# Kernel optimization log

Measured on AMD Instinct MI355X. Metric: run time of the kernel, lower is better.

## Reference

```python
import jax, jax.numpy as jnp
import numpy as np

K = 9  # kernel_size ** 2
G = 4  # groups
POINTS = np.array([[-1, -1], [-1, 0], [-1, 1], [0, -1], [0, 0], [0, 1], [1, -1], [1, 0], [1, 1]], dtype=np.float32)


def conv2d(x, w, b=None, pad=0):
    out = jax.lax.conv_general_dilated(x, w, (1, 1), [(pad, pad), (pad, pad)],
                                       dimension_numbers=('NCHW', 'OIHW', 'NCHW'))
    if b is not None:
        out = out + b[None, :, None, None]
    return out


def pconv(z, w):
    # partial conv: 3x3 conv on first dim//4 channels, rest untouched
    dc = w.shape[0]
    z1 = conv2d(z[:, :dc], w, pad=1)
    return jnp.concatenate([z1, z[:, dc:]], axis=1)


def warp(img, flow):
    # img: (b, Cg, H, W); flow: (b, 2K, H, W) -> (b, Cg, K, H, W)
    # bilinear grid_sample, padding_mode='border', align_corners=True
    b, Cg, H, W = img.shape
    fl = flow.reshape(b, K, 2, H, W)
    gy, gx = jnp.meshgrid(jnp.arange(H, dtype=img.dtype), jnp.arange(W, dtype=img.dtype), indexing='ij')
    px = jnp.clip(gx[None, None] + fl[:, :, 0], 0.0, W - 1)  # (b, K, H, W)
    py = jnp.clip(gy[None, None] + fl[:, :, 1], 0.0, H - 1)
    x0 = jnp.floor(px)
    y0 = jnp.floor(py)
    wx = (px - x0)[:, None]  # (b, 1, K, H, W)
    wy = (py - y0)[:, None]
    x0i = x0.astype(jnp.int32)
    y0i = y0.astype(jnp.int32)
    x1i = jnp.minimum(x0i + 1, W - 1)
    y1i = jnp.minimum(y0i + 1, H - 1)
    gather = jax.vmap(lambda im, iy, ix: im[:, iy, ix])  # per-batch: (Cg,H,W),(K,H,W)->(Cg,K,H,W)
    v00 = gather(img, y0i, x0i)
    v01 = gather(img, y0i, x1i)
    v10 = gather(img, y1i, x0i)
    v11 = gather(img, y1i, x1i)
    return v00 * (1 - wx) * (1 - wy) + v01 * wx * (1 - wy) + v10 * (1 - wx) * wy + v11 * wx * wy


def forward(x, y, off_pconv_w, off_w, off_b, mask_pconv_w, mask_w, mask_b):
    mask = conv2d(pconv(x, mask_pconv_w), mask_w, mask_b)[:, None]  # (b, 1, K, h, w)
    y1, y2 = jnp.split(y, 2, axis=0)
    Cg = y1.shape[1] // G
    pts = jnp.asarray(POINTS).astype(x.dtype)
    outs1, outs2 = [], []
    for i in range(G):
        base = (pts * (2 * i + 1)).reshape(-1)  # (2K,) base offsets at scale 2i+1
        off = conv2d(pconv(x, off_pconv_w[i]), off_w[i], off_b[i]) + base[None, :, None, None]
        outs1.append(warp(y1[:, i * Cg:(i + 1) * Cg], off) * mask)
        outs2.append(warp(y2[:, i * Cg:(i + 1) * Cg], off) * mask)
    return jnp.concatenate([jnp.concatenate(outs1, 1), jnp.concatenate(outs2, 1)], axis=0)


def setup_inputs() -> dict:
    key = jax.random.key(0)
    ks = jax.random.split(key, 8)
    b, inc, H, W = 2, 64, 256, 256
    dc = inc // 4
    return {
        'x': jax.random.normal(ks[0], (b, inc, H, W), jnp.float32),
        'y': jax.random.normal(ks[1], (2 * b, inc, H, W), jnp.float32),
        'off_pconv_w': jax.random.normal(ks[2], (G, dc, dc, 3, 3), jnp.float32) * 0.05,
        'off_w': jax.random.normal(ks[3], (G, 2 * K, inc, 1, 1), jnp.float32) * 0.05,
        'off_b': jax.random.normal(ks[4], (G, 2 * K), jnp.float32) * 0.05,
        'mask_pconv_w': jax.random.normal(ks[5], (dc, dc, 3, 3), jnp.float32) * 0.05,
        'mask_w': jax.random.normal(ks[6], (K, inc, 1, 1), jnp.float32) * 0.05,
        'mask_b': jax.random.normal(ks[7], (K,), jnp.float32) * 0.05,
    }


def reference(x, y, off_pconv_w, off_w, off_b, mask_pconv_w, mask_w, mask_b):
    return forward(x, y, off_pconv_w, off_w, off_b, mask_pconv_w, mask_w, mask_b)
```

## Files before the change

### kernel.cpp

```cpp
#include <hip/hip_runtime.h>

#define HW 65536
#define NOUT 81
#define NFEAT 192
#define WROW 84

typedef unsigned short ushort_t;
typedef unsigned int uint_t;

__device__ __forceinline__ float bf2f(ushort_t u) {
    union { unsigned int i; float f; } v; v.i = ((unsigned int)u) << 16; return v.f;
}
__device__ __forceinline__ float bfhi(uint_t u) {
    union { unsigned int i; float f; } v; v.i = u & 0xffff0000u; return v.f;
}
__device__ __forceinline__ float bflo(uint_t u) {
    union { unsigned int i; float f; } v; v.i = u << 16; return v.f;
}
__device__ __forceinline__ ushort_t f2bf(float f) {
    union { float f; unsigned int i; } v; v.f = f;
    unsigned int r = v.i + 0x7FFF + ((v.i >> 16) & 1);
    return (ushort_t)(r >> 16);
}

__global__ __launch_bounds__(256) void setup_weights(
    const float* __restrict__ off_pconv_w,
    const float* __restrict__ off_w,
    const float* __restrict__ off_b,
    const float* __restrict__ mask_pconv_w,
    const float* __restrict__ mask_w,
    const float* __restrict__ mask_b,
    float* __restrict__ WtP,
    float* __restrict__ biasP)
{
    int id = blockIdx.x * 256 + threadIdx.x;
    const float PTS[18] = {-1,-1, -1,0, -1,1, 0,-1, 0,0, 0,1, 1,-1, 1,0, 1,1};
    if (id < NFEAT * WROW) {
        int f = id / WROW;
        int o = id % WROW;
        float v = 0.f;
        if (o < NOUT) {
            if (f < 144) {
                int p = f >> 4, c = f & 15;
                float s = 0.f;
                if (o < 9) {
                    for (int cm = 0; cm < 16; ++cm)
                        s += mask_w[o * 64 + cm] * mask_pconv_w[(cm * 16 + c) * 9 + p];
                } else {
                    int oo = o - 9, i = oo / 18, j = oo % 18;
                    for (int cm = 0; cm < 16; ++cm)
                        s += off_w[(i * 18 + j) * 64 + cm] * off_pconv_w[((i * 16 + cm) * 16 + c) * 9 + p];
                }
                v = s;
            } else {
                int c = f - 144;
                if (o < 9) v = mask_w[o * 64 + 16 + c];
                else { int oo = o - 9, i = oo / 18, j = oo % 18; v = off_w[(i * 18 + j) * 64 + 16 + c]; }
            }
        }
        WtP[id] = v;
    } else if (id < NFEAT * WROW + NOUT) {
        int o = id - NFEAT * WROW;
        float v;
        if (o < 9) v = mask_b[o];
        else {
            int oo = o - 9, i = oo / 18, j = oo % 18;
            v = off_b[i * 18 + j] + PTS[j] * (float)(2 * i + 1);
        }
        biasP[o] = v;
    }
}

#define FMA21X4(X0, X1, X2, X3, WR) do {                                   \
    _Pragma("unroll")                                                      \
    for (int j5 = 0; j5 < 5; ++j5) {                                       \
        float4 w4 = *(const float4*)((WR) + 4 * j5);                       \
        acc0[4*j5+0] = fmaf(X0, w4.x, acc0[4*j5+0]);                       \
        acc0[4*j5+1] = fmaf(X0, w4.y, acc0[4*j5+1]);                       \
        acc0[4*j5+2] = fmaf(X0, w4.z, acc0[4*j5+2]);                       \
        acc0[4*j5+3] = fmaf(X0, w4.w, acc0[4*j5+3]);                       \
        acc1[4*j5+0] = fmaf(X1, w4.x, acc1[4*j5+0]);                       \
        acc1[4*j5+1] = fmaf(X1, w4.y, acc1[4*j5+1]);                       \
        acc1[4*j5+2] = fmaf(X1, w4.z, acc1[4*j5+2]);                       \
        acc1[4*j5+3] = fmaf(X1, w4.w, acc1[4*j5+3]);                       \
        acc2[4*j5+0] = fmaf(X2, w4.x, acc2[4*j5+0]);                       \
        acc2[4*j5+1] = fmaf(X2, w4.y, acc2[4*j5+1]);                       \
        acc2[4*j5+2] = fmaf(X2, w4.z, acc2[4*j5+2]);                       \
        acc2[4*j5+3] = fmaf(X2, w4.w, acc2[4*j5+3]);                       \
        acc3[4*j5+0] = fmaf(X3, w4.x, acc3[4*j5+0]);                       \
        acc3[4*j5+1] = fmaf(X3, w4.y, acc3[4*j5+1]);                       \
        acc3[4*j5+2] = fmaf(X3, w4.z, acc3[4*j5+2]);                       \
        acc3[4*j5+3] = fmaf(X3, w4.w, acc3[4*j5+3]);                       \
    }                                                                      \
    {                                                                      \
        float w20 = (WR)[20];                                              \
        acc0[20] = fmaf(X0, w20, acc0[20]);                                \
        acc1[20] = fmaf(X1, w20, acc1[20]);                                \
        acc2[20] = fmaf(X2, w20, acc2[20]);                                \
        acc3[20] = fmaf(X3, w20, acc3[20]);                                \
    }                                                                      \
} while (0)

__global__ __launch_bounds__(256, 2) void conv_px4(
    const float* __restrict__ x,
    const float* __restrict__ WtP,
    const float* __restrict__ biasP,
    float* __restrict__ mask_ws,
    float* __restrict__ off_ws)
{
    __shared__ float wl[NFEAT * WROW];
    int tid = threadIdx.x;
    {
        const float4* src = (const float4*)WtP;
        float4* dst = (float4*)wl;
        for (int idx = tid; idx < NFEAT * WROW / 4; idx += 256) dst[idx] = src[idx];
    }
    __syncthreads();

    int c4 = tid & 3, grp = tid >> 2;
    int bid = blockIdx.x;
    int b = bid >> 8, h = bid & 255;
    int wbase = grp * 4;
    int pix0 = h * 256 + wbase;
    int ob0 = c4 * 20;

    float acc0[21], acc1[21], acc2[21], acc3[21];
#pragma unroll
    for (int j = 0; j < 21; ++j) {
        float bj = biasP[ob0 + j];
        acc0[j] = bj; acc1[j] = bj; acc2[j] = bj; acc3[j] = bj;
    }

    const float* xb = x + (size_t)b * 64 * HW;

#pragma unroll 1
    for (int r = 0; r < 3; ++r) {
        int hh = h + r - 1;
        bool vrow = ((unsigned)hh < 256u);
        int rbase = hh * 256 + wbase;
#pragma unroll 1
        for (int c = 0; c < 16; ++c) {
            const float* xr = xb + c * HW + rbase;
            float4 x4 = vrow ? *(const float4*)xr : make_float4(0.f, 0.f, 0.f, 0.f);
            float xm1 = (vrow && wbase > 0)       ? xr[-1] : 0.f;
            float xp4 = (vrow && wbase + 4 < 256) ? xr[4]  : 0.f;
            const float* wr0 = wl + ((r * 3 + 0) * 16 + c) * WROW + ob0;
            const float* wr1 = wl + ((r * 3 + 1) * 16 + c) * WROW + ob0;
            const float* wr2 = wl + ((r * 3 + 2) * 16 + c) * WROW + ob0;
            FMA21X4(xm1, x4.x, x4.y, x4.z, wr0);
            FMA21X4(x4.x, x4.y, x4.z, x4.w, wr1);
            FMA21X4(x4.y, x4.z, x4.w, xp4, wr2);
        }
    }
#pragma unroll 1
    for (int c = 0; c < 48; ++c) {
        float4 x4 = *(const float4*)(xb + (16 + c) * HW + pix0);
        const float* wr = wl + (144 + c) * WROW + ob0;
        FMA21X4(x4.x, x4.y, x4.z, x4.w, wr);
    }

#pragma unroll
    for (int j = 0; j < 21; ++j) {
        int o = ob0 + j;
        float* pl;
        if (o < 9) pl = mask_ws + (size_t)(b * 9 + o) * HW + pix0;
        else       pl = off_ws  + (size_t)(b * 72 + (o - 9)) * HW + pix0;
        pl[0] = acc0[j];
        pl[1] = acc1[j];
        pl[2] = acc2[j];
        pl[3] = acc3[j];
    }
}

__global__ __launch_bounds__(256) void transpose_y_c(
    const float* __restrict__ y, ushort_t* __restrict__ Tc)
{
    int bid = blockIdx.x;
    int z = bid & 7, pr = bid >> 3;
    int pix = pr * 256 + threadIdx.x;
    int xb = z >> 2, i = z & 3;

    const float* p0 = y + (size_t)(xb * 64 + i * 16) * HW + pix;
    const float* p1 = y + (size_t)((xb + 2) * 64 + i * 16) * HW + pix;

    ushort_t v0[16], v1[16];
#pragma unroll
    for (int c = 0; c < 16; ++c) v0[c] = f2bf(p0[(size_t)c * HW]);
#pragma unroll
    for (int c = 0; c < 16; ++c) v1[c] = f2bf(p1[(size_t)c * HW]);

    uint4* dst = (uint4*)(Tc + ((size_t)z * HW + pix) * 32);
#pragma unroll
    for (int j = 0; j < 4; ++j) {
        ushort_t row[8] = {v0[4*j], v0[4*j+1], v0[4*j+2], v0[4*j+3],
                           v1[4*j], v1[4*j+1], v1[4*j+2], v1[4*j+3]};
        dst[j] = *(const uint4*)row;
    }
}

__global__ __launch_bounds__(256) void warp_apply_c(
    const ushort_t* __restrict__ Tc,
    const float* __restrict__ mask_ws,
    const float* __restrict__ off_ws,
    float* __restrict__ out)
{
    int bid = blockIdx.x;
    int z  = bid & 7;
    int wc = (bid >> 3) & 3;
    int h  = bid >> 5;
    int c4 = threadIdx.x & 3;
    int pl = threadIdx.x >> 2;
    int w  = wc * 64 + pl;
    int pix = h * 256 + w;
    int xb = z >> 2, i = z & 3;

    const ushort_t* Tt = Tc + (size_t)z * HW * 32;

    float oxv[9], oyv[9], mv[9];
#pragma unroll
    for (int k = 0; k < 9; ++k) {
        oxv[k] = off_ws[(size_t)(z * 18 + 2 * k) * HW + pix];
        oyv[k] = off_ws[(size_t)(z * 18 + 2 * k + 1) * HW + pix];
        mv[k]  = mask_ws[(size_t)(xb * 9 + k) * HW + pix];
    }

    float* ob0 = out + ((size_t)(xb * 64 + i * 16 + c4 * 4)) * 9 * HW + pix;
    float* ob1 = ob0 + (size_t)128 * 9 * HW;
    int sec = c4 * 8;

#pragma unroll 1
    for (int k = 0; k < 9; ++k) {
        float m = mv[k];
        float px = fminf(fmaxf((float)w + oxv[k], 0.f), 255.f);
        float py = fminf(fmaxf((float)h + oyv[k], 0.f), 255.f);
        float x0f = floorf(px), y0f = floorf(py);
        float wx = px - x0f, wy = py - y0f;
        int x0 = (int)x0f, y0 = (int)y0f;
        int x1 = min(x0 + 1, 255), y1 = min(y0 + 1, 255);

        float w00 = (1.f - wx) * (1.f - wy) * m;
        float w01 = wx * (1.f - wy) * m;
        float w10 = (1.f - wx) * wy * m;
        float w11 = wx * wy * m;

        uint4 A = *(const uint4*)(Tt + (size_t)(y0 * 256 + x0) * 32 + sec);
        uint4 B = *(const uint4*)(Tt + (size_t)(y0 * 256 + x1) * 32 + sec);
        uint4 C = *(const uint4*)(Tt + (size_t)(y1 * 256 + x0) * 32 + sec);
        uint4 D = *(const uint4*)(Tt + (size_t)(y1 * 256 + x1) * 32 + sec);

        float s0 = w00 * bflo(A.x), s1 = w00 * bfhi(A.x);
        float s2 = w00 * bflo(A.y), s3 = w00 * bfhi(A.y);
        float u0 = w00 * bflo(A.z), u1 = w00 * bfhi(A.z);
        float u2 = w00 * bflo(A.w), u3 = w00 * bfhi(A.w);

        s0 = fmaf(w01, bflo(B.x), s0); s1 = fmaf(w01, bfhi(B.x), s1);
        s2 = fmaf(w01, bflo(B.y), s2); s3 = fmaf(w01, bfhi(B.y), s3);
        u0 = fmaf(w01, bflo(B.z), u0); u1 = fmaf(w01, bfhi(B.z), u1);
        u2 = fmaf(w01, bflo(B.w), u2); u3 = fmaf(w01, bfhi(B.w), u3);

        s0 = fmaf(w10, bflo(C.x), s0); s1 = fmaf(w10, bfhi(C.x), s1);
        s2 = fmaf(w10, bflo(C.y), s2); s3 = fmaf(w10, bfhi(C.y), s3);
        u0 = fmaf(w10, bflo(C.z), u0); u1 = fmaf(w10, bfhi(C.z), u1);
        u2 = fmaf(w10, bflo(C.w), u2); u3 = fmaf(w10, bfhi(C.w), u3);

        s0 = fmaf(w11, bflo(D.x), s0); s1 = fmaf(w11, bfhi(D.x), s1);
        s2 = fmaf(w11, bflo(D.y), s2); s3 = fmaf(w11, bfhi(D.y), s3);
        u0 = fmaf(w11, bflo(D.z), u0); u1 = fmaf(w11, bfhi(D.z), u1);
        u2 = fmaf(w11, bflo(D.w), u2); u3 = fmaf(w11, bfhi(D.w), u3);

        float* p0 = ob0 + (size_t)k * HW;
        __builtin_nontemporal_store(s0, p0);
        __builtin_nontemporal_store(s1, p0 + (size_t)9 * HW);
        __builtin_nontemporal_store(s2, p0 + (size_t)18 * HW);
        __builtin_nontemporal_store(s3, p0 + (size_t)27 * HW);
        float* p1 = ob1 + (size_t)k * HW;
        __builtin_nontemporal_store(u0, p1);
        __builtin_nontemporal_store(u1, p1 + (size_t)9 * HW);
        __builtin_nontemporal_store(u2, p1 + (size_t)18 * HW);
        __builtin_nontemporal_store(u3, p1 + (size_t)27 * HW);
    }
}

__global__ __launch_bounds__(512) void conv_offsets_lds(
    const float* __restrict__ x, const float* __restrict__ WtP,
    const float* __restrict__ biasP,
    float* __restrict__ mask_ws, float* __restrict__ off_ws)
{
    __shared__ float wl[NFEAT * WROW + NOUT];
    int tid = threadIdx.x;
    for (int idx = tid; idx < NFEAT * WROW; idx += 512) wl[idx] = WtP[idx];
    if (tid < NOUT) wl[NFEAT * WROW + tid] = biasP[tid];
    __syncthreads();

    int gid = blockIdx.x * 512 + tid;
    int b = gid >> 16;
    int pix = gid & 65535;
    int h = pix >> 8, w = pix & 255;

    float acc[NOUT];
#pragma unroll
    for (int o = 0; o < NOUT; ++o) acc[o] = wl[NFEAT * WROW + o];

    const float* xb = x + (size_t)b * 64 * HW;
    for (int p = 0; p < 9; ++p) {
        int hh = h + p / 3 - 1;
        int ww = w + p % 3 - 1;
        bool valid = ((unsigned)hh < 256u) && ((unsigned)ww < 256u);
        int poff = hh * 256 + ww;
        for (int c = 0; c < 16; ++c) {
            float xv = valid ? xb[c * HW + poff] : 0.f;
            const float* wr = &wl[(p * 16 + c) * WROW];
#pragma unroll
            for (int o = 0; o < NOUT; ++o) acc[o] = fmaf(xv, wr[o], acc[o]);
        }
    }
    for (int c = 0; c < 48; ++c) {
        float xv = xb[(16 + c) * HW + pix];
        const float* wr = &wl[(144 + c) * WROW];
#pragma unroll
        for (int o = 0; o < NOUT; ++o) acc[o] = fmaf(xv, wr[o], acc[o]);
    }
#pragma unroll
    for (int k = 0; k < 9; ++k) mask_ws[(b * 9 + k) * HW + pix] = acc[k];
#pragma unroll
    for (int t = 0; t < 72; ++t) off_ws[(b * 72 + t) * HW + pix] = acc[9 + t];
}

__global__ __launch_bounds__(256) void warp_apply(
    const float* __restrict__ y,
    const float* __restrict__ mask_ws,
    const float* __restrict__ off_ws,
    float* __restrict__ out)
{
    int w = threadIdx.x;
    int h = blockIdx.x;
    int k = blockIdx.y;
    int z = blockIdx.z;
    int xb = z >> 2, i = z & 3;
    int pix = h * 256 + w;

    float ox = off_ws[(size_t)(z * 18 + 2 * k) * HW + pix];
    float oy = off_ws[(size_t)(z * 18 + 2 * k + 1) * HW + pix];
    float m  = mask_ws[(size_t)(xb * 9 + k) * HW + pix];

    float px = fminf(fmaxf((float)w + ox, 0.f), 255.f);
    float py = fminf(fmaxf((float)h + oy, 0.f), 255.f);
    float x0f = floorf(px), y0f = floorf(py);
    float wx = px - x0f, wy = py - y0f;
    int x0 = (int)x0f, y0 = (int)y0f;
    int x1 = min(x0 + 1, 255), y1 = min(y0 + 1, 255);

    float w00 = (1.f - wx) * (1.f - wy) * m;
    float w01 = wx * (1.f - wy) * m;
    float w10 = (1.f - wx) * wy * m;
    float w11 = wx * wy * m;

    int o00 = y0 * 256 + x0, o01 = y0 * 256 + x1;
    int o10 = y1 * 256 + x0, o11 = y1 * 256 + x1;

    const float* p1 = y + (size_t)(xb * 64 + i * 16) * HW;
    const float* p2 = y + (size_t)((xb + 2) * 64 + i * 16) * HW;
    float* out1 = out + ((size_t)(xb * 64 + i * 16) * 9 + k) * HW + pix;
    float* out2 = out + ((size_t)((xb + 2) * 64 + i * 16) * 9 + k) * HW + pix;

#pragma unroll
    for (int c = 0; c < 16; ++c) {
        const float* q = p1 + (size_t)c * HW;
        float v = w00 * q[o00] + w01 * q[o01] + w10 * q[o10] + w11 * q[o11];
        out1[(size_t)c * 9 * HW] = v;
        q = p2 + (size_t)c * HW;
        v = w00 * q[o00] + w01 * q[o01] + w10 * q[o10] + w11 * q[o11];
        out2[(size_t)c * 9 * HW] = v;
    }
}

extern "C" void kernel_launch(void* const* d_in, const int* in_sizes, int n_in,
                              void* d_out, int out_size, void* d_ws, size_t ws_size,
                              hipStream_t stream) {
    const float* x            = (const float*)d_in[0];
    const float* y            = (const float*)d_in[1];
    const float* off_pconv_w  = (const float*)d_in[2];
    const float* off_w        = (const float*)d_in[3];
    const float* off_b        = (const float*)d_in[4];
    const float* mask_pconv_w = (const float*)d_in[5];
    const float* mask_w       = (const float*)d_in[6];
    const float* mask_b       = (const float*)d_in[7];
    float* out = (float*)d_out;

    float* WtP     = (float*)d_ws;
    float* biasP   = WtP + NFEAT * WROW;
    float* mask_ws = (float*)((char*)d_ws + 65536);
    float* off_ws  = mask_ws + (size_t)2 * 9 * HW;
    ushort_t* Tc   = (ushort_t*)(off_ws + (size_t)2 * 72 * HW);
    size_t need = 65536 + (size_t)2 * 9 * HW * 4 + (size_t)2 * 72 * HW * 4
                + (size_t)8 * HW * 32 * 2;

    setup_weights<<<64, 256, 0, stream>>>(off_pconv_w, off_w, off_b,
                                          mask_pconv_w, mask_w, mask_b, WtP, biasP);

    if (ws_size >= need) {
        conv_px4<<<512, 256, 0, stream>>>(x, WtP, biasP, mask_ws, off_ws);
        transpose_y_c<<<2048, 256, 0, stream>>>(y, Tc);
        warp_apply_c<<<8192, 256, 0, stream>>>(Tc, mask_ws, off_ws, out);
    } else {
        conv_offsets_lds<<<256, 512, 0, stream>>>(x, WtP, biasP, mask_ws, off_ws);
        dim3 g2(256, 9, 8);
        warp_apply<<<g2, 256, 0, stream>>>(y, mask_ws, off_ws, out);
    }
}
```

Baseline: 299.6 us.

## Replace LDS-tiled offset conv with wave-uniform scalar-load weight conv

Replaces the conv kernel, which staged weights in LDS and gave each thread 4 pixels × 21 outputs, with one where each wavefront handles 64 pixels and a wave-uniform 21-output slice. The slice index goes through readfirstlane so the compiler can read weights from global memory with scalar loads. This drops the LDS staging, the barrier and LDS read traffic, and raises occupancy through smaller register use. In exchange each input pixel is loaded four times, once per output slice wave, with no float4 reuse across neighbouring pixels. The unused LDS fallback conv kernel is removed.

```diff
diff --git a/kernel.cpp b/kernel.cpp
--- a/kernel.cpp
+++ b/kernel.cpp
@@ -8,9 +8,6 @@
 typedef unsigned short ushort_t;
 typedef unsigned int uint_t;
 
-__device__ __forceinline__ float bf2f(ushort_t u) {
-    union { unsigned int i; float f; } v; v.i = ((unsigned int)u) << 16; return v.f;
-}
 __device__ __forceinline__ float bfhi(uint_t u) {
     union { unsigned int i; float f; } v; v.i = u & 0xffff0000u; return v.f;
 }
@@ -71,104 +68,59 @@
     }
 }
 
-#define FMA21X4(X0, X1, X2, X3, WR) do {                                   \
-    _Pragma("unroll")                                                      \
-    for (int j5 = 0; j5 < 5; ++j5) {                                       \
-        float4 w4 = *(const float4*)((WR) + 4 * j5);                       \
-        acc0[4*j5+0] = fmaf(X0, w4.x, acc0[4*j5+0]);                       \
-        acc0[4*j5+1] = fmaf(X0, w4.y, acc0[4*j5+1]);                       \
-        acc0[4*j5+2] = fmaf(X0, w4.z, acc0[4*j5+2]);                       \
-        acc0[4*j5+3] = fmaf(X0, w4.w, acc0[4*j5+3]);                       \
-        acc1[4*j5+0] = fmaf(X1, w4.x, acc1[4*j5+0]);                       \
-        acc1[4*j5+1] = fmaf(X1, w4.y, acc1[4*j5+1]);                       \
-        acc1[4*j5+2] = fmaf(X1, w4.z, acc1[4*j5+2]);                       \
-        acc1[4*j5+3] = fmaf(X1, w4.w, acc1[4*j5+3]);                       \
-        acc2[4*j5+0] = fmaf(X2, w4.x, acc2[4*j5+0]);                       \
-        acc2[4*j5+1] = fmaf(X2, w4.y, acc2[4*j5+1]);                       \
-        acc2[4*j5+2] = fmaf(X2, w4.z, acc2[4*j5+2]);                       \
-        acc2[4*j5+3] = fmaf(X2, w4.w, acc2[4*j5+3]);                       \
-        acc3[4*j5+0] = fmaf(X3, w4.x, acc3[4*j5+0]);                       \
-        acc3[4*j5+1] = fmaf(X3, w4.y, acc3[4*j5+1]);                       \
-        acc3[4*j5+2] = fmaf(X3, w4.z, acc3[4*j5+2]);                       \
-        acc3[4*j5+3] = fmaf(X3, w4.w, acc3[4*j5+3]);                       \
-    }                                                                      \
-    {                                                                      \
-        float w20 = (WR)[20];                                              \
-        acc0[20] = fmaf(X0, w20, acc0[20]);                                \
-        acc1[20] = fmaf(X1, w20, acc1[20]);                                \
-        acc2[20] = fmaf(X2, w20, acc2[20]);                                \
-        acc3[20] = fmaf(X3, w20, acc3[20]);                                \
-    }                                                                      \
-} while (0)
-
-__global__ __launch_bounds__(256, 2) void conv_px4(
+__global__ __launch_bounds__(256) void conv_sgpr(
     const float* __restrict__ x,
     const float* __restrict__ WtP,
     const float* __restrict__ biasP,
     float* __restrict__ mask_ws,
     float* __restrict__ off_ws)
 {
-    __shared__ float wl[NFEAT * WROW];
     int tid = threadIdx.x;
-    {
-        const float4* src = (const float4*)WtP;
-        float4* dst = (float4*)wl;
-        for (int idx = tid; idx < NFEAT * WROW / 4; idx += 256) dst[idx] = src[idx];
-    }
-    __syncthreads();
-
-    int c4 = tid & 3, grp = tid >> 2;
+    int lane = tid & 63;
     int bid = blockIdx.x;
-    int b = bid >> 8, h = bid & 255;
-    int wbase = grp * 4;
-    int pix0 = h * 256 + wbase;
-    int ob0 = c4 * 20;
-
-    float acc0[21], acc1[21], acc2[21], acc3[21];
-#pragma unroll
-    for (int j = 0; j < 21; ++j) {
-        float bj = biasP[ob0 + j];
-        acc0[j] = bj; acc1[j] = bj; acc2[j] = bj; acc3[j] = bj;
-    }
+    int b = bid >> 10;
+    int pixblk = (bid & 1023) * 64;
+    int pix = pixblk + lane;
+    int h = pix >> 8, w = pix & 255;
+
+    int ob0 = __builtin_amdgcn_readfirstlane((tid >> 6) * 20);
+
+    float acc[21];
+#pragma unroll
+    for (int j = 0; j < 21; ++j) acc[j] = biasP[ob0 + j];
 
     const float* xb = x + (size_t)b * 64 * HW;
 
 #pragma unroll 1
-    for (int r = 0; r < 3; ++r) {
-        int hh = h + r - 1;
-        bool vrow = ((unsigned)hh < 256u);
-        int rbase = hh * 256 + wbase;
+    for (int p = 0; p < 9; ++p) {
+        int hh = h + p / 3 - 1;
+        int dx = p % 3 - 1;
+        int ww = w + dx;
+        bool valid = ((unsigned)hh < 256u) && ((unsigned)ww < 256u);
+        int poff = hh * 256 + ww;
 #pragma unroll 1
         for (int c = 0; c < 16; ++c) {
-            const float* xr = xb + c * HW + rbase;
-            float4 x4 = vrow ? *(const float4*)xr : make_float4(0.f, 0.f, 0.f, 0.f);
-            float xm1 = (vrow && wbase > 0)       ? xr[-1] : 0.f;
-            float xp4 = (vrow && wbase + 4 < 256) ? xr[4]  : 0.f;
-            const float* wr0 = wl + ((r * 3 + 0) * 16 + c) * WROW + ob0;
-            const float* wr1 = wl + ((r * 3 + 1) * 16 + c) * WROW + ob0;
-            const float* wr2 = wl + ((r * 3 + 2) * 16 + c) * WROW + ob0;
-            FMA21X4(xm1, x4.x, x4.y, x4.z, wr0);
-            FMA21X4(x4.x, x4.y, x4.z, x4.w, wr1);
-            FMA21X4(x4.y, x4.z, x4.w, xp4, wr2);
+            float xv = valid ? xb[c * HW + poff] : 0.f;
+            const float* wr = WtP + (p * 16 + c) * WROW + ob0;
+#pragma unroll
+            for (int j = 0; j < 21; ++j) acc[j] = fmaf(xv, wr[j], acc[j]);
         }
     }
 #pragma unroll 1
     for (int c = 0; c < 48; ++c) {
-        float4 x4 = *(const float4*)(xb + (16 + c) * HW + pix0);
-        const float* wr = wl + (144 + c) * WROW + ob0;
-        FMA21X4(x4.x, x4.y, x4.z, x4.w, wr);
+        float xv = xb[(16 + c) * HW + pix];
+        const float* wr = WtP + (144 + c) * WROW + ob0;
+#pragma unroll
+        for (int j = 0; j < 21; ++j) acc[j] = fmaf(xv, wr[j], acc[j]);
     }
 
 #pragma unroll
     for (int j = 0; j < 21; ++j) {
         int o = ob0 + j;
         float* pl;
-        if (o < 9) pl = mask_ws + (size_t)(b * 9 + o) * HW + pix0;
-        else       pl = off_ws  + (size_t)(b * 72 + (o - 9)) * HW + pix0;
-        pl[0] = acc0[j];
-        pl[1] = acc1[j];
-        pl[2] = acc2[j];
-        pl[3] = acc3[j];
+        if (o < 9) pl = mask_ws + (size_t)(b * 9 + o) * HW + pix;
+        else       pl = off_ws  + (size_t)(b * 72 + (o - 9)) * HW + pix;
+        *pl = acc[j];
     }
 }
 
@@ -279,51 +231,6 @@
         __builtin_nontemporal_store(u2, p1 + (size_t)18 * HW);
         __builtin_nontemporal_store(u3, p1 + (size_t)27 * HW);
     }
-}
-
-__global__ __launch_bounds__(512) void conv_offsets_lds(
-    const float* __restrict__ x, const float* __restrict__ WtP,
-    const float* __restrict__ biasP,
-    float* __restrict__ mask_ws, float* __restrict__ off_ws)
-{
-    __shared__ float wl[NFEAT * WROW + NOUT];
-    int tid = threadIdx.x;
-    for (int idx = tid; idx < NFEAT * WROW; idx += 512) wl[idx] = WtP[idx];
-    if (tid < NOUT) wl[NFEAT * WROW + tid] = biasP[tid];
-    __syncthreads();
-
-    int gid = blockIdx.x * 512 + tid;
-    int b = gid >> 16;
-    int pix = gid & 65535;
-    int h = pix >> 8, w = pix & 255;
-
-    float acc[NOUT];
-#pragma unroll
-    for (int o = 0; o < NOUT; ++o) acc[o] = wl[NFEAT * WROW + o];
-
-    const float* xb = x + (size_t)b * 64 * HW;
-    for (int p = 0; p < 9; ++p) {
-        int hh = h + p / 3 - 1;
-        int ww = w + p % 3 - 1;
-        bool valid = ((unsigned)hh < 256u) && ((unsigned)ww < 256u);
-        int poff = hh * 256 + ww;
-        for (int c = 0; c < 16; ++c) {
-            float xv = valid ? xb[c * HW + poff] : 0.f;
-            const float* wr = &wl[(p * 16 + c) * WROW];
-#pragma unroll
-            for (int o = 0; o < NOUT; ++o) acc[o] = fmaf(xv, wr[o], acc[o]);
-        }
-    }
-    for (int c = 0; c < 48; ++c) {
-        float xv = xb[(16 + c) * HW + pix];
-        const float* wr = &wl[(144 + c) * WROW];
-#pragma unroll
-        for (int o = 0; o < NOUT; ++o) acc[o] = fmaf(xv, wr[o], acc[o]);
-    }
-#pragma unroll
-    for (int k = 0; k < 9; ++k) mask_ws[(b * 9 + k) * HW + pix] = acc[k];
-#pragma unroll
-    for (int t = 0; t < 72; ++t) off_ws[(b * 72 + t) * HW + pix] = acc[9 + t];
 }
 
 __global__ __launch_bounds__(256) void warp_apply(
@@ -398,12 +305,12 @@
     setup_weights<<<64, 256, 0, stream>>>(off_pconv_w, off_w, off_b,
                                           mask_pconv_w, mask_w, mask_b, WtP, biasP);
 
+    conv_sgpr<<<2048, 256, 0, stream>>>(x, WtP, biasP, mask_ws, off_ws);
+
     if (ws_size >= need) {
-        conv_px4<<<512, 256, 0, stream>>>(x, WtP, biasP, mask_ws, off_ws);
         transpose_y_c<<<2048, 256, 0, stream>>>(y, Tc);
         warp_apply_c<<<8192, 256, 0, stream>>>(Tc, mask_ws, off_ws, out);
     } else {
-        conv_offsets_lds<<<256, 512, 0, stream>>>(x, WtP, biasP, mask_ws, off_ws);
         dim3 g2(256, 9, 8);
         warp_apply<<<g2, 256, 0, stream>>>(y, mask_ws, off_ws, out);
     }
```

Measured after the change: 295.0 us. No clear change (-1.5%).
